# Performance work log

Measured on AMD Instinct MI355X. Metric: run time of the kernel, lower is better.

## Reference

```python
import jax, jax.numpy as jnp
import numpy as np

N_NODES = 100000
N_EDGES = 1600000
DIM = 128
N_LAYERS = 3
N_GRAPHS = 128
OUT = 2


def setup_inputs() -> dict:
    key = jax.random.key(0)
    ks = jax.random.split(key, 8)
    x = jax.random.normal(ks[0], (N_NODES, DIM), dtype=jnp.float32)
    edge_index = jax.random.randint(ks[1], (2, N_EDGES), 0, N_NODES, dtype=jnp.int32)
    batch = jnp.sort(jax.random.randint(ks[2], (N_NODES,), 0, N_GRAPHS, dtype=jnp.int32))
    s = 1.0 / np.sqrt(DIM)
    conv_w = jax.random.normal(ks[3], (N_LAYERS, DIM, DIM), dtype=jnp.float32) * s
    conv_b = jnp.zeros((N_LAYERS, DIM), dtype=jnp.float32)
    lin1_w = jax.random.normal(ks[4], (DIM, DIM), dtype=jnp.float32) * s
    lin1_b = jnp.zeros((DIM,), dtype=jnp.float32)
    lin2_w = jax.random.normal(ks[5], (DIM, OUT), dtype=jnp.float32) * s
    lin2_b = jnp.zeros((OUT,), dtype=jnp.float32)
    return {"x": x, "edge_index": edge_index, "batch": batch,
            "conv_w": conv_w, "conv_b": conv_b,
            "lin1_w": lin1_w, "lin1_b": lin1_b,
            "lin2_w": lin2_w, "lin2_b": lin2_b}


def _gcn_conv(x, src, dst, norm, w, b, n_nodes):
    # linear transform first (in==out==DIM), then gather-scale-scatter
    h = x @ w                                    # [N, dim]
    msg = h[src] * norm[:, None]                 # [E+N, dim] gathered messages
    out = jax.ops.segment_sum(msg, dst, num_segments=n_nodes)
    return out + b


def reference(x, edge_index, batch, conv_w, conv_b, lin1_w, lin1_b, lin2_w, lin2_b):
    n = x.shape[0]
    loop = jnp.arange(n, dtype=edge_index.dtype)
    src = jnp.concatenate([edge_index[0], loop])  # PyG: add self-loops
    dst = jnp.concatenate([edge_index[1], loop])
    # symmetric normalization: deg computed on destination (col) with self-loops
    deg = jax.ops.segment_sum(jnp.ones_like(dst, dtype=x.dtype), dst, num_segments=n)
    deg_inv_sqrt = jnp.where(deg > 0, jax.lax.rsqrt(jnp.maximum(deg, 1.0)), 0.0)
    norm = deg_inv_sqrt[src] * deg_inv_sqrt[dst]

    h = x
    for i in range(conv_w.shape[0]):  # fixed small layer count
        h = jax.nn.relu(_gcn_conv(h, src, dst, norm, conv_w[i], conv_b[i], n))

    # global mean pool over graphs in the batch
    sums = jax.ops.segment_sum(h, batch, num_segments=N_GRAPHS)
    cnts = jax.ops.segment_sum(jnp.ones((n,), dtype=h.dtype), batch, num_segments=N_GRAPHS)
    g = sums / jnp.maximum(cnts, 1.0)[:, None]   # [G, dim]

    g = jax.nn.relu(g @ lin1_w + lin1_b)
    # dropout is inference-mode identity (training=False)
    logits = g @ lin2_w + lin2_b
    return jax.nn.log_softmax(logits, axis=-1)
```

## Files before the change

kernel.cpp:

```cpp
#include <hip/hip_runtime.h>
#include <hip/hip_fp16.h>
#include <math.h>

#define DIM 128
#define BINSH 10
#define EPB 8192
#define PAD 18432

typedef __attribute__((ext_vector_type(8))) _Float16 half8;
typedef __attribute__((ext_vector_type(4))) float f32x4;
typedef __attribute__((ext_vector_type(2))) float f32x2;

__global__ __launch_bounds__(256) void prep_k(const float* __restrict__ conv_w,
                                              _Float16* __restrict__ bp,
                                              int* __restrict__ bincur, int nbc) {
    int g = blockIdx.x * 256 + threadIdx.x;
    if (g < nbc) bincur[g] = 0;
    if (g >= 3 * 2048) return;
    int l = g >> 11;
    int rem = g & 2047;
    int c = rem >> 8;
    int f = (rem >> 6) & 3;
    int lane = rem & 63;
    const float* W = conv_w + l * DIM * DIM;
    int kbase = f * 32 + (lane >> 4) * 8;
    int col = c * 16 + (lane & 15);
    _Float16* d = bp + ((size_t)l * 2048 + (size_t)(c * 4 + f) * 64 + lane) * 8;
#pragma unroll
    for (int j = 0; j < 8; ++j)
        d[j] = (_Float16)W[(kbase + j) * DIM + col];
}

__global__ __launch_bounds__(1024) void bin_k(const int* __restrict__ src,
                                              const int* __restrict__ dst,
                                              int* __restrict__ bincur,
                                              unsigned int* __restrict__ tmp,
                                              int E, int NBIN) {
    __shared__ int cur[128];
    const int t = threadIdx.x;
    if (t < 128) cur[t] = 0;
    __syncthreads();
    const int e0 = blockIdx.x * EPB;
    const int e1 = min(e0 + EPB, E);
    for (int e = e0 + t; e < e1; e += 1024)
        atomicAdd(&cur[dst[e] >> BINSH], 1);
    __syncthreads();
    if (t < NBIN) {
        int h = cur[t];
        cur[t] = h ? atomicAdd(&bincur[t * 16], h) : 0;
    }
    __syncthreads();
    for (int e = e0 + t; e < e1; e += 1024) {
        int d = dst[e], s = src[e];
        int b = d >> BINSH;
        int pos = atomicAdd(&cur[b], 1);
        if (pos < PAD)
            tmp[(size_t)b * PAD + pos] =
                (unsigned int)((s << BINSH) | (d & ((1 << BINSH) - 1)));
    }
}

__global__ __launch_bounds__(1024) void fused_k(const unsigned int* __restrict__ tmp,
                                                const int* __restrict__ bincur,
                                                int2* __restrict__ rowse,
                                                float* __restrict__ dis,
                                                int* __restrict__ ew, int n) {
    __shared__ unsigned int led[PAD];
    __shared__ int cnt[1 << BINSH];
    __shared__ int lcur[1 << BINSH];
    const int b = blockIdx.x, t = threadIdx.x;
    const int size = min(bincur[b * 16], PAD);
    const unsigned int* bt = tmp + (size_t)b * PAD;
    cnt[t] = 0;
    for (int e = t; e < size; e += 1024) led[e] = bt[e];
    __syncthreads();
    for (int e = t; e < size; e += 1024)
        atomicAdd(&cnt[led[e] & ((1 << BINSH) - 1)], 1);
    __syncthreads();
    int v = cnt[t];
    __syncthreads();
    for (int off = 1; off < 1024; off <<= 1) {
        int u = (t >= off) ? cnt[t - off] : 0;
        __syncthreads();
        cnt[t] += u;
        __syncthreads();
    }
    int start = b * PAD + cnt[t] - v;
    lcur[t] = start;
    int node = (b << BINSH) + t;
    if (node < n) {
        rowse[node] = make_int2(start, start + v);
        dis[node] = rsqrtf((float)(v + 1));
    }
    __syncthreads();
    for (int e = t; e < size; e += 1024) {
        unsigned int u = led[e];
        int q = atomicAdd(&lcur[u & ((1 << BINSH) - 1)], 1);
        ew[q] = (int)(u >> BINSH);
    }
}

template <bool FP16IN>
__global__ __launch_bounds__(256) void gemm_k(const void* __restrict__ Ain,
                                              const _Float16* __restrict__ Bp,
                                              const float* __restrict__ dis,
                                              unsigned int* __restrict__ T32, int n) {
    const int t = threadIdx.x;
    const int lane = t & 63;
    const int wave = t >> 6;
    const int quad = lane >> 4;
    const int m    = lane & 15;
    const int row  = blockIdx.x * 64 + wave * 16 + m;
    const bool act = row < n;

    half8 a[4];
    float dvr = 0.f;
    if (act) {
        dvr = dis[row];
        if (FP16IN) {
            const _Float16* A = (const _Float16*)Ain + (size_t)row * DIM;
#pragma unroll
            for (int f = 0; f < 4; ++f)
                a[f] = *(const half8*)(A + f * 32 + quad * 8);
        } else {
            const float* A = (const float*)Ain + (size_t)row * DIM;
#pragma unroll
            for (int f = 0; f < 4; ++f) {
                float4 v0 = *(const float4*)(A + f * 32 + quad * 8);
                float4 v1 = *(const float4*)(A + f * 32 + quad * 8 + 4);
                __half2 h01 = __floats2half2_rn(v0.x, v0.y);
                __half2 h23 = __floats2half2_rn(v0.z, v0.w);
                __half2 h45 = __floats2half2_rn(v1.x, v1.y);
                __half2 h67 = __floats2half2_rn(v1.z, v1.w);
                int4 pk;
                pk.x = *(int*)&h01; pk.y = *(int*)&h23;
                pk.z = *(int*)&h45; pk.w = *(int*)&h67;
                a[f] = *(half8*)&pk;
            }
        }
    } else {
#pragma unroll
        for (int f = 0; f < 4; ++f) a[f] = half8{};
    }

    const half8* B8 = (const half8*)Bp;
#pragma unroll
    for (int c = 0; c < 8; ++c) {
        f32x4 acc = {0.f, 0.f, 0.f, 0.f};
#pragma unroll
        for (int f = 0; f < 4; ++f) {
            half8 b = B8[(c * 4 + f) * 64 + lane];
            acc = __builtin_amdgcn_mfma_f32_16x16x32_f16(b, a[f], acc, 0, 0, 0);
        }
        if (act) {
            int r = 0;
            r = __builtin_amdgcn_cvt_pk_fp8_f32(dvr * acc[0], dvr * acc[1], r, 0);
            r = __builtin_amdgcn_cvt_pk_fp8_f32(dvr * acc[2], dvr * acc[3], r, 1);
            T32[(size_t)row * 32 + c * 4 + quad] = (unsigned int)r;
        }
    }
}

#define ACC_EDGE(rr) { \
    f32x2 a0 = __builtin_amdgcn_cvt_pk_f32_fp8((int)rr.x, 0); \
    f32x2 a1 = __builtin_amdgcn_cvt_pk_f32_fp8((int)rr.x, 1); \
    f32x2 a2 = __builtin_amdgcn_cvt_pk_f32_fp8((int)rr.y, 0); \
    f32x2 a3 = __builtin_amdgcn_cvt_pk_f32_fp8((int)rr.y, 1); \
    acc[0] += a0[0]; acc[1] += a0[1]; \
    acc[2] += a1[0]; acc[3] += a1[1]; \
    acc[4] += a2[0]; acc[5] += a2[1]; \
    acc[6] += a3[0]; acc[7] += a3[1]; }

__global__ __launch_bounds__(256) void agg_k(const unsigned int* __restrict__ T32,
                                             const int2* __restrict__ rowse,
                                             const int* __restrict__ ew,
                                             const float* __restrict__ dis,
                                             const float* __restrict__ bias,
                                             __half* __restrict__ O, int n) {
    const int lane = threadIdx.x & 63;
    const int li   = lane & 15;
    const int v = blockIdx.x * 16 + (threadIdx.x >> 6) * 4 + (lane >> 4);
    const bool act = v < n;

    const uint2* T2 = (const uint2*)T32;

    int e0 = 0, e1 = 0;
    float dv = 0.f;
    if (act) {
        int2 re = rowse[v];
        e0 = re.x; e1 = re.y;
        dv = dis[v];
    }

    float acc[8] = {0.f, 0.f, 0.f, 0.f, 0.f, 0.f, 0.f, 0.f};

    if (act) {
        uint2 rs = T2[(size_t)v * 16 + li];
        ACC_EDGE(rs);
    }

    int e = e0;
    for (; e + 8 <= e1; e += 8) {
        int c0 = ew[e + 0], c1 = ew[e + 1], c2 = ew[e + 2], c3 = ew[e + 3];
        int c4 = ew[e + 4], c5 = ew[e + 5], c6 = ew[e + 6], c7 = ew[e + 7];
        uint2 r0 = T2[(size_t)c0 * 16 + li];
        uint2 r1 = T2[(size_t)c1 * 16 + li];
        uint2 r2 = T2[(size_t)c2 * 16 + li];
        uint2 r3 = T2[(size_t)c3 * 16 + li];
        uint2 r4 = T2[(size_t)c4 * 16 + li];
        uint2 r5 = T2[(size_t)c5 * 16 + li];
        uint2 r6 = T2[(size_t)c6 * 16 + li];
        uint2 r7 = T2[(size_t)c7 * 16 + li];
        ACC_EDGE(r0); ACC_EDGE(r1); ACC_EDGE(r2); ACC_EDGE(r3);
        ACC_EDGE(r4); ACC_EDGE(r5); ACC_EDGE(r6); ACC_EDGE(r7);
    }
    for (; e + 4 <= e1; e += 4) {
        int c0 = ew[e + 0], c1 = ew[e + 1], c2 = ew[e + 2], c3 = ew[e + 3];
        uint2 r0 = T2[(size_t)c0 * 16 + li];
        uint2 r1 = T2[(size_t)c1 * 16 + li];
        uint2 r2 = T2[(size_t)c2 * 16 + li];
        uint2 r3 = T2[(size_t)c3 * 16 + li];
        ACC_EDGE(r0); ACC_EDGE(r1); ACC_EDGE(r2); ACC_EDGE(r3);
    }
    for (; e + 2 <= e1; e += 2) {
        int c0 = ew[e + 0], c1 = ew[e + 1];
        uint2 r0 = T2[(size_t)c0 * 16 + li];
        uint2 r1 = T2[(size_t)c1 * 16 + li];
        ACC_EDGE(r0); ACC_EDGE(r1);
    }
    if (e < e1) {
        uint2 r0 = T2[(size_t)ew[e] * 16 + li];
        ACC_EDGE(r0);
    }

    if (act) {
        float4 b0 = ((const float4*)bias)[li * 2 + 0];
        float4 b1 = ((const float4*)bias)[li * 2 + 1];
        __half2 o0 = __floats2half2_rn(fmaxf(dv * acc[0] + b0.x, 0.f),
                                       fmaxf(dv * acc[1] + b0.y, 0.f));
        __half2 o1 = __floats2half2_rn(fmaxf(dv * acc[2] + b0.z, 0.f),
                                       fmaxf(dv * acc[3] + b0.w, 0.f));
        __half2 o2 = __floats2half2_rn(fmaxf(dv * acc[4] + b1.x, 0.f),
                                       fmaxf(dv * acc[5] + b1.y, 0.f));
        __half2 o3 = __floats2half2_rn(fmaxf(dv * acc[6] + b1.z, 0.f),
                                       fmaxf(dv * acc[7] + b1.w, 0.f));
        int4 o;
        o.x = *(int*)&o0; o.y = *(int*)&o1; o.z = *(int*)&o2; o.w = *(int*)&o3;
        *(int4*)(O + (size_t)v * DIM + li * 8) = o;
    }
}

__global__ __launch_bounds__(1024) void poolhead_k(const __half* __restrict__ H,
                                                   const int* __restrict__ batch,
                                                   const float* __restrict__ l1w,
                                                   const float* __restrict__ l1b,
                                                   const float* __restrict__ l2w,
                                                   const float* __restrict__ l2b,
                                                   float* __restrict__ out, int n) {
    const int g = blockIdx.x, t = threadIdx.x;
    const int g8 = t >> 4;
    const int li = t & 15;
    __shared__ float red[1024 * 8];
    __shared__ float gs[128];

    int lo = 0, hi = n;
    while (lo < hi) { int m = (lo + hi) >> 1; if (batch[m] < g) lo = m + 1; else hi = m; }
    int start = lo;
    lo = start; hi = n;
    while (lo < hi) { int m = (lo + hi) >> 1; if (batch[m] < g + 1) lo = m + 1; else hi = m; }
    int end = lo;
    int cnt = end - start;

    float s[8] = {0.f, 0.f, 0.f, 0.f, 0.f, 0.f, 0.f, 0.f};
    for (int v = start + g8; v < end; v += 64) {
        int4 pk = *((const int4*)(H + (size_t)v * DIM) + li);
        const __half2* h2 = (const __half2*)&pk;
#pragma unroll
        for (int j = 0; j < 4; ++j) {
            float2 f = __half22float2(h2[j]);
            s[2 * j + 0] += f.x;
            s[2 * j + 1] += f.y;
        }
    }
#pragma unroll
    for (int j = 0; j < 8; ++j) red[t * 8 + j] = s[j];
    __syncthreads();
    for (int st = 32; st > 0; st >>= 1) {
        if (g8 < st) {
#pragma unroll
            for (int j = 0; j < 8; ++j)
                red[t * 8 + j] += red[(t + st * 16) * 8 + j];
        }
        __syncthreads();
    }
    if (t < 16) {
        float inv = cnt > 0 ? 1.f / (float)cnt : 0.f;
#pragma unroll
        for (int j = 0; j < 8; ++j) gs[t * 8 + j] = red[t * 8 + j] * inv;
    }
    __syncthreads();

    float y = 0.f;
    if (t < 128) {
        float acc = l1b[t];
        for (int k = 0; k < 128; ++k) acc += gs[k] * l1w[k * 128 + t];
        y = fmaxf(acc, 0.f);
    }
    float2* red2 = (float2*)red;
    if (t < 128) red2[t] = make_float2(y * l2w[t * 2 + 0], y * l2w[t * 2 + 1]);
    __syncthreads();
    for (int sfd = 64; sfd > 0; sfd >>= 1) {
        if (t < sfd) {
            red2[t].x += red2[t + sfd].x;
            red2[t].y += red2[t + sfd].y;
        }
        __syncthreads();
    }
    if (t == 0) {
        float l0 = red2[0].x + l2b[0];
        float l1 = red2[0].y + l2b[1];
        float m = fmaxf(l0, l1);
        float lse = m + logf(expf(l0 - m) + expf(l1 - m));
        out[g * 2 + 0] = l0 - lse;
        out[g * 2 + 1] = l1 - lse;
    }
}

extern "C" void kernel_launch(void* const* d_in, const int* in_sizes, int n_in,
                              void* d_out, int out_size, void* d_ws, size_t ws_size,
                              hipStream_t stream) {
    const float* x       = (const float*)d_in[0];
    const int*   ei      = (const int*)d_in[1];
    const int*   batch   = (const int*)d_in[2];
    const float* conv_w  = (const float*)d_in[3];
    const float* conv_b  = (const float*)d_in[4];
    const float* lin1_w  = (const float*)d_in[5];
    const float* lin1_b  = (const float*)d_in[6];
    const float* lin2_w  = (const float*)d_in[7];
    const float* lin2_b  = (const float*)d_in[8];
    float* out = (float*)d_out;

    const int n = in_sizes[0] / DIM;
    const int E = in_sizes[1] / 2;
    const int n_graphs = 128;
    const int NBIN = (n + (1 << BINSH) - 1) >> BINSH;

    const int* src = ei;
    const int* dst = ei + E;

    char* p = (char*)d_ws;
    auto alloc = [&](size_t bytes) {
        char* r = p;
        p += (bytes + 255) & ~(size_t)255;
        return r;
    };
    __half*        bufH    = (__half*)alloc((size_t)n * DIM * 2);
    unsigned int*  bufT    = (unsigned int*)alloc((size_t)n * DIM);
    float*         dis     = (float*)alloc((size_t)n * 4);
    int2*          rowse   = (int2*)alloc((size_t)n * 8);
    int*           bincur  = (int*)alloc((size_t)NBIN * 16 * 4);
    unsigned int*  tmp     = (unsigned int*)alloc((size_t)NBIN * PAD * 4);
    int*           ew      = (int*)alloc((size_t)NBIN * PAD * 4);
    _Float16*      bp      = (_Float16*)alloc((size_t)3 * 2048 * 8 * 2);
    (void)ws_size;

    const int binBlocks = (E + EPB - 1) / EPB;

    prep_k<<<24, 256, 0, stream>>>(conv_w, bp, bincur, NBIN * 16);
    bin_k<<<binBlocks, 1024, 0, stream>>>(src, dst, bincur, tmp, E, NBIN);
    fused_k<<<NBIN, 1024, 0, stream>>>(tmp, bincur, rowse, dis, ew, n);

    const int gemmBlocks = (n + 63) / 64;
    const int aggBlocks = (n + 15) / 16;

    gemm_k<false><<<gemmBlocks, 256, 0, stream>>>((const void*)x, bp + 0 * 16384, dis, bufT, n);
    agg_k<<<aggBlocks, 256, 0, stream>>>(bufT, rowse, ew, dis, conv_b + 0 * DIM, bufH, n);
    gemm_k<true><<<gemmBlocks, 256, 0, stream>>>((const void*)bufH, bp + 1 * 16384, dis, bufT, n);
    agg_k<<<aggBlocks, 256, 0, stream>>>(bufT, rowse, ew, dis, conv_b + 1 * DIM, bufH, n);
    gemm_k<true><<<gemmBlocks, 256, 0, stream>>>((const void*)bufH, bp + 2 * 16384, dis, bufT, n);
    agg_k<<<aggBlocks, 256, 0, stream>>>(bufT, rowse, ew, dis, conv_b + 2 * DIM, bufH, n);

    poolhead_k<<<n_graphs, 1024, 0, stream>>>(bufH, batch, lin1_w, lin1_b, lin2_w, lin2_b, out, n);
}
```

Before: 310.6 us.

## Fuse aggregation with next layer's GEMM via LDS tile, ping-pong fp8 buffers

Layers 1 and 2 now aggregate 64 nodes per block into an fp16 tile in shared memory, then run the next layer's MFMA transform on that tile and write fp8 output directly. This removes the fp16 intermediate write and read and two kernel launches. The fp8 buffers are double-buffered so a kernel never reads the buffer it writes. In exchange, each block processes 64 nodes in four serial sub-passes plus a barrier, which cuts the parallelism available to hide gather latency.

```diff
diff --git a/kernel.cpp b/kernel.cpp
--- a/kernel.cpp
+++ b/kernel.cpp
@@ -6,6 +6,7 @@
 #define BINSH 10
 #define EPB 8192
 #define PAD 18432
+#define ALH 136
 
 typedef __attribute__((ext_vector_type(8))) _Float16 half8;
 typedef __attribute__((ext_vector_type(4))) float f32x4;
@@ -100,67 +101,6 @@
     }
 }
 
-template <bool FP16IN>
-__global__ __launch_bounds__(256) void gemm_k(const void* __restrict__ Ain,
-                                              const _Float16* __restrict__ Bp,
-                                              const float* __restrict__ dis,
-                                              unsigned int* __restrict__ T32, int n) {
-    const int t = threadIdx.x;
-    const int lane = t & 63;
-    const int wave = t >> 6;
-    const int quad = lane >> 4;
-    const int m    = lane & 15;
-    const int row  = blockIdx.x * 64 + wave * 16 + m;
-    const bool act = row < n;
-
-    half8 a[4];
-    float dvr = 0.f;
-    if (act) {
-        dvr = dis[row];
-        if (FP16IN) {
-            const _Float16* A = (const _Float16*)Ain + (size_t)row * DIM;
-#pragma unroll
-            for (int f = 0; f < 4; ++f)
-                a[f] = *(const half8*)(A + f * 32 + quad * 8);
-        } else {
-            const float* A = (const float*)Ain + (size_t)row * DIM;
-#pragma unroll
-            for (int f = 0; f < 4; ++f) {
-                float4 v0 = *(const float4*)(A + f * 32 + quad * 8);
-                float4 v1 = *(const float4*)(A + f * 32 + quad * 8 + 4);
-                __half2 h01 = __floats2half2_rn(v0.x, v0.y);
-                __half2 h23 = __floats2half2_rn(v0.z, v0.w);
-                __half2 h45 = __floats2half2_rn(v1.x, v1.y);
-                __half2 h67 = __floats2half2_rn(v1.z, v1.w);
-                int4 pk;
-                pk.x = *(int*)&h01; pk.y = *(int*)&h23;
-                pk.z = *(int*)&h45; pk.w = *(int*)&h67;
-                a[f] = *(half8*)&pk;
-            }
-        }
-    } else {
-#pragma unroll
-        for (int f = 0; f < 4; ++f) a[f] = half8{};
-    }
-
-    const half8* B8 = (const half8*)Bp;
-#pragma unroll
-    for (int c = 0; c < 8; ++c) {
-        f32x4 acc = {0.f, 0.f, 0.f, 0.f};
-#pragma unroll
-        for (int f = 0; f < 4; ++f) {
-            half8 b = B8[(c * 4 + f) * 64 + lane];
-            acc = __builtin_amdgcn_mfma_f32_16x16x32_f16(b, a[f], acc, 0, 0, 0);
-        }
-        if (act) {
-            int r = 0;
-            r = __builtin_amdgcn_cvt_pk_fp8_f32(dvr * acc[0], dvr * acc[1], r, 0);
-            r = __builtin_amdgcn_cvt_pk_fp8_f32(dvr * acc[2], dvr * acc[3], r, 1);
-            T32[(size_t)row * 32 + c * 4 + quad] = (unsigned int)r;
-        }
-    }
-}
-
 #define ACC_EDGE(rr) { \
     f32x2 a0 = __builtin_amdgcn_cvt_pk_f32_fp8((int)rr.x, 0); \
     f32x2 a1 = __builtin_amdgcn_cvt_pk_f32_fp8((int)rr.x, 1); \
@@ -171,34 +111,9 @@
     acc[4] += a2[0]; acc[5] += a2[1]; \
     acc[6] += a3[0]; acc[7] += a3[1]; }
 
-__global__ __launch_bounds__(256) void agg_k(const unsigned int* __restrict__ T32,
-                                             const int2* __restrict__ rowse,
-                                             const int* __restrict__ ew,
-                                             const float* __restrict__ dis,
-                                             const float* __restrict__ bias,
-                                             __half* __restrict__ O, int n) {
-    const int lane = threadIdx.x & 63;
-    const int li   = lane & 15;
-    const int v = blockIdx.x * 16 + (threadIdx.x >> 6) * 4 + (lane >> 4);
-    const bool act = v < n;
-
-    const uint2* T2 = (const uint2*)T32;
-
-    int e0 = 0, e1 = 0;
-    float dv = 0.f;
-    if (act) {
-        int2 re = rowse[v];
-        e0 = re.x; e1 = re.y;
-        dv = dis[v];
-    }
-
-    float acc[8] = {0.f, 0.f, 0.f, 0.f, 0.f, 0.f, 0.f, 0.f};
-
-    if (act) {
-        uint2 rs = T2[(size_t)v * 16 + li];
-        ACC_EDGE(rs);
-    }
-
+__device__ __forceinline__ void agg_edges(const uint2* __restrict__ T2,
+                                          const int* __restrict__ ew,
+                                          int e0, int e1, int li, float* acc) {
     int e = e0;
     for (; e + 8 <= e1; e += 8) {
         int c0 = ew[e + 0], c1 = ew[e + 1], c2 = ew[e + 2], c3 = ew[e + 3];
@@ -232,6 +147,174 @@
         uint2 r0 = T2[(size_t)ew[e] * 16 + li];
         ACC_EDGE(r0);
     }
+}
+
+__global__ __launch_bounds__(256) void gemm_k(const float* __restrict__ Ain,
+                                              const _Float16* __restrict__ Bp,
+                                              const float* __restrict__ dis,
+                                              unsigned int* __restrict__ T32, int n) {
+    const int t = threadIdx.x;
+    const int lane = t & 63;
+    const int wave = t >> 6;
+    const int quad = lane >> 4;
+    const int m    = lane & 15;
+    const int row  = blockIdx.x * 64 + wave * 16 + m;
+    const bool act = row < n;
+
+    half8 a[4];
+    float dvr = 0.f;
+    if (act) {
+        dvr = dis[row];
+        const float* A = Ain + (size_t)row * DIM;
+#pragma unroll
+        for (int f = 0; f < 4; ++f) {
+            float4 v0 = *(const float4*)(A + f * 32 + quad * 8);
+            float4 v1 = *(const float4*)(A + f * 32 + quad * 8 + 4);
+            __half2 h01 = __floats2half2_rn(v0.x, v0.y);
+            __half2 h23 = __floats2half2_rn(v0.z, v0.w);
+            __half2 h45 = __floats2half2_rn(v1.x, v1.y);
+            __half2 h67 = __floats2half2_rn(v1.z, v1.w);
+            int4 pk;
+            pk.x = *(int*)&h01; pk.y = *(int*)&h23;
+            pk.z = *(int*)&h45; pk.w = *(int*)&h67;
+            a[f] = *(half8*)&pk;
+        }
+    } else {
+#pragma unroll
+        for (int f = 0; f < 4; ++f) a[f] = half8{};
+    }
+
+    const half8* B8 = (const half8*)Bp;
+#pragma unroll
+    for (int c = 0; c < 8; ++c) {
+        f32x4 acc = {0.f, 0.f, 0.f, 0.f};
+#pragma unroll
+        for (int f = 0; f < 4; ++f) {
+            half8 b = B8[(c * 4 + f) * 64 + lane];
+            acc = __builtin_amdgcn_mfma_f32_16x16x32_f16(b, a[f], acc, 0, 0, 0);
+        }
+        if (act) {
+            int r = 0;
+            r = __builtin_amdgcn_cvt_pk_fp8_f32(dvr * acc[0], dvr * acc[1], r, 0);
+            r = __builtin_amdgcn_cvt_pk_fp8_f32(dvr * acc[2], dvr * acc[3], r, 1);
+            T32[(size_t)row * 32 + c * 4 + quad] = (unsigned int)r;
+        }
+    }
+}
+
+__global__ __launch_bounds__(256) void aggemm_k(const unsigned int* __restrict__ Tin,
+                                                const int2* __restrict__ rowse,
+                                                const int* __restrict__ ew,
+                                                const float* __restrict__ dis,
+                                                const float* __restrict__ bias,
+                                                const _Float16* __restrict__ Bp,
+                                                unsigned int* __restrict__ Tout,
+                                                int n) {
+    __shared__ _Float16 Al[64 * ALH];
+    const int lane = threadIdx.x & 63;
+    const int wv   = threadIdx.x >> 6;
+    const int li   = lane & 15;
+    const int qd   = lane >> 4;
+    const int r0   = blockIdx.x * 64;
+    const uint2* T2 = (const uint2*)Tin;
+
+    float4 b0 = ((const float4*)bias)[li * 2 + 0];
+    float4 b1 = ((const float4*)bias)[li * 2 + 1];
+
+#pragma unroll
+    for (int sub = 0; sub < 4; ++sub) {
+        const int lrow = sub * 16 + wv * 4 + qd;
+        const int v = r0 + lrow;
+        const bool act = v < n;
+        int e0 = 0, e1 = 0;
+        float dv = 0.f;
+        if (act) {
+            int2 re = rowse[v];
+            e0 = re.x; e1 = re.y;
+            dv = dis[v];
+        }
+        float acc[8] = {0.f, 0.f, 0.f, 0.f, 0.f, 0.f, 0.f, 0.f};
+        if (act) {
+            uint2 rs = T2[(size_t)v * 16 + li];
+            ACC_EDGE(rs);
+        }
+        agg_edges(T2, ew, e0, e1, li, acc);
+
+        __half2 o0 = __floats2half2_rn(fmaxf(dv * acc[0] + b0.x, 0.f),
+                                       fmaxf(dv * acc[1] + b0.y, 0.f));
+        __half2 o1 = __floats2half2_rn(fmaxf(dv * acc[2] + b0.z, 0.f),
+                                       fmaxf(dv * acc[3] + b0.w, 0.f));
+        __half2 o2 = __floats2half2_rn(fmaxf(dv * acc[4] + b1.x, 0.f),
+                                       fmaxf(dv * acc[5] + b1.y, 0.f));
+        __half2 o3 = __floats2half2_rn(fmaxf(dv * acc[6] + b1.z, 0.f),
+                                       fmaxf(dv * acc[7] + b1.w, 0.f));
+        int4 o;
+        if (act) {
+            o.x = *(int*)&o0; o.y = *(int*)&o1; o.z = *(int*)&o2; o.w = *(int*)&o3;
+        } else {
+            o = make_int4(0, 0, 0, 0);
+        }
+        *(int4*)&Al[lrow * ALH + li * 8] = o;
+    }
+    __syncthreads();
+
+    const int quad = lane >> 4;
+    const int m    = lane & 15;
+    const int lrow = wv * 16 + m;
+    const int row  = r0 + lrow;
+    const bool act = row < n;
+
+    half8 a[4];
+#pragma unroll
+    for (int f = 0; f < 4; ++f)
+        a[f] = *(const half8*)&Al[lrow * ALH + f * 32 + quad * 8];
+    float dvr = act ? dis[row] : 0.f;
+
+    const half8* B8 = (const half8*)Bp;
+#pragma unroll
+    for (int c = 0; c < 8; ++c) {
+        f32x4 acc = {0.f, 0.f, 0.f, 0.f};
+#pragma unroll
+        for (int f = 0; f < 4; ++f) {
+            half8 b = B8[(c * 4 + f) * 64 + lane];
+            acc = __builtin_amdgcn_mfma_f32_16x16x32_f16(b, a[f], acc, 0, 0, 0);
+        }
+        if (act) {
+            int r = 0;
+            r = __builtin_amdgcn_cvt_pk_fp8_f32(dvr * acc[0], dvr * acc[1], r, 0);
+            r = __builtin_amdgcn_cvt_pk_fp8_f32(dvr * acc[2], dvr * acc[3], r, 1);
+            Tout[(size_t)row * 32 + c * 4 + quad] = (unsigned int)r;
+        }
+    }
+}
+
+__global__ __launch_bounds__(256) void agg_k(const unsigned int* __restrict__ T32,
+                                             const int2* __restrict__ rowse,
+                                             const int* __restrict__ ew,
+                                             const float* __restrict__ dis,
+                                             const float* __restrict__ bias,
+                                             __half* __restrict__ O, int n) {
+    const int lane = threadIdx.x & 63;
+    const int li   = lane & 15;
+    const int v = blockIdx.x * 16 + (threadIdx.x >> 6) * 4 + (lane >> 4);
+    const bool act = v < n;
+
+    const uint2* T2 = (const uint2*)T32;
+
+    int e0 = 0, e1 = 0;
+    float dv = 0.f;
+    if (act) {
+        int2 re = rowse[v];
+        e0 = re.x; e1 = re.y;
+        dv = dis[v];
+    }
+
+    float acc[8] = {0.f, 0.f, 0.f, 0.f, 0.f, 0.f, 0.f, 0.f};
+    if (act) {
+        uint2 rs = T2[(size_t)v * 16 + li];
+        ACC_EDGE(rs);
+    }
+    agg_edges(T2, ew, e0, e1, li, acc);
 
     if (act) {
         float4 b0 = ((const float4*)bias)[li * 2 + 0];
@@ -355,7 +438,8 @@
         return r;
     };
     __half*        bufH    = (__half*)alloc((size_t)n * DIM * 2);
-    unsigned int*  bufT    = (unsigned int*)alloc((size_t)n * DIM);
+    unsigned int*  bufT0   = (unsigned int*)alloc((size_t)n * DIM);
+    unsigned int*  bufT1   = (unsigned int*)alloc((size_t)n * DIM);
     float*         dis     = (float*)alloc((size_t)n * 4);
     int2*          rowse   = (int2*)alloc((size_t)n * 8);
     int*           bincur  = (int*)alloc((size_t)NBIN * 16 * 4);
@@ -370,15 +454,15 @@
     bin_k<<<binBlocks, 1024, 0, stream>>>(src, dst, bincur, tmp, E, NBIN);
     fused_k<<<NBIN, 1024, 0, stream>>>(tmp, bincur, rowse, dis, ew, n);
 
-    const int gemmBlocks = (n + 63) / 64;
-    const int aggBlocks = (n + 15) / 16;
-
-    gemm_k<false><<<gemmBlocks, 256, 0, stream>>>((const void*)x, bp + 0 * 16384, dis, bufT, n);
-    agg_k<<<aggBlocks, 256, 0, stream>>>(bufT, rowse, ew, dis, conv_b + 0 * DIM, bufH, n);
-    gemm_k<true><<<gemmBlocks, 256, 0, stream>>>((const void*)bufH, bp + 1 * 16384, dis, bufT, n);
-    agg_k<<<aggBlocks, 256, 0, stream>>>(bufT, rowse, ew, dis, conv_b + 1 * DIM, bufH, n);
-    gemm_k<true><<<gemmBlocks, 256, 0, stream>>>((const void*)bufH, bp + 2 * 16384, dis, bufT, n);
-    agg_k<<<aggBlocks, 256, 0, stream>>>(bufT, rowse, ew, dis, conv_b + 2 * DIM, bufH, n);
+    const int tileBlocks = (n + 63) / 64;
+    const int aggBlocks  = (n + 15) / 16;
+
+    gemm_k<<<tileBlocks, 256, 0, stream>>>(x, bp + 0 * 16384, dis, bufT0, n);
+    aggemm_k<<<tileBlocks, 256, 0, stream>>>(bufT0, rowse, ew, dis,
+                                             conv_b + 0 * DIM, bp + 1 * 16384, bufT1, n);
+    aggemm_k<<<tileBlocks, 256, 0, stream>>>(bufT1, rowse, ew, dis,
+                                             conv_b + 1 * DIM, bp + 2 * 16384, bufT0, n);
+    agg_k<<<aggBlocks, 256, 0, stream>>>(bufT0, rowse, ew, dis, conv_b + 2 * DIM, bufH, n);
 
     poolhead_k<<<n_graphs, 1024, 0, stream>>>(bufH, batch, lin1_w, lin1_b, lin2_w, lin2_b, out, n);
 }
```

Measured after the change: 312.2 us. No clear change (+0.5%).
